# Kernel optimization log

Measured on AMD Instinct MI355X. Metric: run time of the kernel, lower is better.

Reference implementation:

```python
import jax, jax.numpy as jnp
import numpy as np

B, S, E, H, F = 4, 1024, 1024, 16, 4096
D = E // H
DEPTH = 3
EPS_LN = 1e-5
EPS_ENT = 1e-6


def setup_inputs() -> dict:
    key = jax.random.key(0)
    ks = jax.random.split(key, 32)
    def w(k, shp, s=0.02):
        return (jax.random.normal(k, shp) * s).astype(jnp.float32)
    z = lambda *shp: jnp.zeros(shp, jnp.float32)
    inp = {
        'x': jax.random.normal(ks[0], (B, S, E), jnp.float32),
        # self-referential attention
        'sr_w': w(ks[1], (E, E)), 'sr_b': z(E),
        'q_w': w(ks[2], (E, E)), 'q_b': z(E),
        'k_w': w(ks[3], (E, E)), 'k_b': z(E),
        'v_w': w(ks[4], (E, E)), 'v_b': z(E),
        'o_w': w(ks[5], (E, E)), 'o_b': z(E),
        'ref_gate': jnp.float32(0.5),
        # quantum-classical interface
        'c_w': w(ks[6], (E, E)), 'c_b': z(E),
        'qp_w': w(ks[7], (E, E)), 'qp_b': z(E),
        'ig_w': w(ks[8], (2 * E, E)), 'ig_b': z(E),
        'temperature': jnp.float32(1.0),
        # entropy regulator
        'kp_w': w(ks[9], (E, E)), 'kp_b': z(E),
        'ee_w': w(ks[10], (E, 1)), 'ee_b': z(1),
        'eta': jnp.float32(0.1),
        # ffn
        'f1_w': w(ks[11], (E, F)), 'f1_b': z(F),
        'f2_w': w(ks[12], (F, E)), 'f2_b': z(E),
        # layernorms
        'ln1_g': jnp.ones(E, jnp.float32), 'ln1_b': z(E),
        'ln2_g': jnp.ones(E, jnp.float32), 'ln2_b': z(E),
        'ln3_g': jnp.ones(E, jnp.float32), 'ln3_b': z(E),
        # observer
        'obs_w': w(ks[13], (E, E)), 'obs_b': z(E),
        'obs_gate': jnp.float32(0.2),
    }
    return inp


def _lin(x, W, b):
    return x @ W + b


def _ln(x, g, b):
    m = jnp.mean(x, -1, keepdims=True)
    v = jnp.var(x, -1, keepdims=True)
    return (x - m) * jax.lax.rsqrt(v + EPS_LN) * g + b


def _layer(x, p):
    ks = jax.lax.stop_gradient(x)  # knowledge_state = x.detach()
    scale = 1.0 / (D ** 0.5)
    for _ in range(DEPTH):  # fixed small recursion depth
        # --- self-referential attention on norm1(x) ---
        xn = _ln(x, p['ln1_g'], p['ln1_b'])
        xr = xn + p['ref_gate'] * _lin(xn, p['sr_w'], p['sr_b'])
        b, s, _ = xn.shape
        q = _lin(xr, p['q_w'], p['q_b']).reshape(b, s, H, D)
        k = _lin(xr, p['k_w'], p['k_b']).reshape(b, s, H, D)
        v = _lin(xn, p['v_w'], p['v_b']).reshape(b, s, H, D)
        scores = jnp.einsum('bqhd,bkhd->bhqk', q, k) * scale  # [B,H,S,S]
        aw = jax.nn.softmax(scores, axis=-1)
        ao = jnp.einsum('bhqk,bkhd->bqhd', aw, v).reshape(b, s, E)
        quantum = _lin(ao, p['o_w'], p['o_b'])
        # --- FFN on norm2(x) (dropout = identity, eval mode) ---
        xn2 = _ln(x, p['ln2_g'], p['ln2_b'])
        h = jax.nn.gelu(_lin(xn2, p['f1_w'], p['f1_b']), approximate=False)
        classical = _lin(h, p['f2_w'], p['f2_b'])
        # --- quantum-classical interface ---
        c_proj = _lin(classical, p['c_w'], p['c_b'])
        q_proj = _lin(quantum, p['qp_w'], p['qp_b'])
        gate = jax.nn.sigmoid(_lin(jnp.concatenate([c_proj, q_proj], -1), p['ig_w'], p['ig_b']))
        sim = jnp.einsum('bqe,bke->bqk', c_proj, q_proj) / (E ** 0.5)  # [B,S,S]
        attw = jax.nn.softmax(sim / p['temperature'], axis=-1)
        transfer = jnp.einsum('bqk,bke->bqe', attw, quantum)
        iface = classical + gate * transfer
        # --- entropy regulator ---
        logp = jax.nn.log_softmax(iface, axis=-1)
        entropy = -jnp.sum(jnp.exp(logp) * logp, -1, keepdims=True)
        neg_entropy = _lin(ks, p['kp_w'], p['kp_b'])
        bal = jax.nn.sigmoid(_lin(iface, p['ee_w'], p['ee_b']))
        regulated = iface + p['eta'] * bal * (neg_entropy / (entropy + EPS_ENT))
        # --- residual + observer feedback + knowledge update ---
        x = x + regulated
        x = x + p['obs_gate'] * _lin(x, p['obs_w'], p['obs_b'])
        ks = ks + 0.1 * (x - ks)
    x = _ln(x, p['ln3_g'], p['ln3_b'])
    return x, ks


def reference(x, sr_w, sr_b, q_w, q_b, k_w, k_b, v_w, v_b, o_w, o_b, ref_gate,
              c_w, c_b, qp_w, qp_b, ig_w, ig_b, temperature,
              kp_w, kp_b, ee_w, ee_b, eta,
              f1_w, f1_b, f2_w, f2_b,
              ln1_g, ln1_b, ln2_g, ln2_b, ln3_g, ln3_b,
              obs_w, obs_b, obs_gate):
    p = dict(sr_w=sr_w, sr_b=sr_b, q_w=q_w, q_b=q_b, k_w=k_w, k_b=k_b,
             v_w=v_w, v_b=v_b, o_w=o_w, o_b=o_b, ref_gate=ref_gate,
             c_w=c_w, c_b=c_b, qp_w=qp_w, qp_b=qp_b, ig_w=ig_w, ig_b=ig_b,
             temperature=temperature, kp_w=kp_w, kp_b=kp_b, ee_w=ee_w, ee_b=ee_b,
             eta=eta, f1_w=f1_w, f1_b=f1_b, f2_w=f2_w, f2_b=f2_b,
             ln1_g=ln1_g, ln1_b=ln1_b, ln2_g=ln2_g, ln2_b=ln2_b,
             ln3_g=ln3_g, ln3_b=ln3_b, obs_w=obs_w, obs_b=obs_b, obs_gate=obs_gate)
    return _layer(x, p)
```

## Files before the change

kernel.cpp:

```cpp
#include <hip/hip_runtime.h>
#include <hip/hip_bf16.h>
#include <cmath>


typedef unsigned short u16;
typedef short v8s __attribute__((ext_vector_type(8)));
typedef float v4f __attribute__((ext_vector_type(4)));
typedef unsigned short u16x4 __attribute__((ext_vector_type(4)));

#define DEV __device__ __forceinline__

DEV float b2f(u16 u) { return __uint_as_float(((unsigned int)u) << 16); }
DEV u16 f2b(float f) {
    unsigned int x = __float_as_uint(f);
    return (u16)((x + 0x7fffu + ((x >> 16) & 1u)) >> 16);
}
DEV bool badf(float f) { return ((__float_as_uint(f) >> 23) & 0xFF) == 0xFF; }

DEV void async16(const void* g, void* l) {
    __builtin_amdgcn_global_load_lds((const __attribute__((address_space(1))) void*)g,
                                     (__attribute__((address_space(3))) void*)l, 16, 0, 0);
}

struct InArr { const void* p[37]; int n[37]; };
struct BJobs { int si[20]; int off[20]; int n[20]; };
struct GJ2 { const u16* jA; const u16* jB; const u16* jbias; u16* jout; };

#define CLS_CAP 131072

__global__ void reset_k(int* diag, int* cnt) {
    if (threadIdx.x == 0) *diag = 0x7FFFFFFF;
    if (threadIdx.x < 80) cnt[threadIdx.x] = 0;
}

__global__ void classify_k(InArr A, int* cnt) {
    int i = blockIdx.y;
    int n = A.n[i];
    if (n <= 1) return;
    const u16* q = (const u16*)A.p[i];
    long pairs = n >> 1;
    int wild = 0, pz = 0;
    if (pairs > (long)CLS_CAP) {
        long chunk = CLS_CAP / gridDim.x;
        long p0 = (long)blockIdx.x * (pairs / gridDim.x);
        for (long j = p0 + threadIdx.x; j < p0 + chunk; j += blockDim.x) {
            u16 w0 = q[2 * j], w1 = q[2 * j + 1];
            wild += ((w0 & 0x7FFF) >= 0x5000) + ((w1 & 0x7FFF) >= 0x5000);
            pz += (w0 == 0 && w1 >= 0x3000 && w1 <= 0x4100) ? 1 : 0;
        }
    } else {
        long stride = (long)gridDim.x * blockDim.x;
        for (long j = (long)blockIdx.x * blockDim.x + threadIdx.x; j < pairs; j += stride) {
            u16 w0 = q[2 * j], w1 = q[2 * j + 1];
            wild += ((w0 & 0x7FFF) >= 0x5000) + ((w1 & 0x7FFF) >= 0x5000);
            pz += (w0 == 0 && w1 >= 0x3000 && w1 <= 0x4100) ? 1 : 0;
        }
    }
#pragma unroll
    for (int off = 1; off < 64; off <<= 1) {
        wild += __shfl_xor(wild, off);
        pz += __shfl_xor(pz, off);
    }
    if ((threadIdx.x & 63) == 0) {
        atomicAdd(&cnt[2 * i], wild);
        atomicAdd(&cnt[2 * i + 1], pz);
    }
}

__global__ void finalize_k(InArr A, const int* cnt, int* flags) {
    int i = threadIdx.x;
    if (i < 37) {
        int n = A.n[i];
        int f = 0;
        if (n > 1) {
            long pairs = (long)n >> 1;
            long wthr, pthr;
            if (pairs > (long)CLS_CAP) { wthr = (2L * CLS_CAP) >> 6; pthr = (long)CLS_CAP >> 2; }
            else { wthr = (long)n >> 6; pthr = (long)n >> 3; }
            f = (cnt[2 * i] > wthr) || (cnt[2 * i + 1] > pthr);
        }
        flags[i] = f;
    }
}

DEV float dec_scalar(const u16* p) {
    float bf = b2f(p[0]);
    if (bf > 0.0009765625f && bf < 8.0f) return bf;
    unsigned int w = (((unsigned int)p[1]) << 16) | (unsigned int)p[0];
    return __uint_as_float(w);
}

__global__ void decode_scalars_k(const u16* rg, const u16* tp, const u16* et,
                                 const u16* og, float* out)
{
    if (threadIdx.x == 0 && blockIdx.x == 0) {
        out[0] = dec_scalar(rg);
        out[1] = dec_scalar(tp);
        out[2] = dec_scalar(et);
        out[3] = dec_scalar(og);
    }
}

__global__ void cvt1d_k(InArr A, BJobs J, const int* flags, u16* BIA) {
    int j = blockIdx.y;
    int n = J.n[j];
    int si = J.si[j];
    const void* src = A.p[si];
    u16* dst = BIA + (long)J.off[j] * 1024;
    int f = flags[si];
    int stride = gridDim.x * blockDim.x;
    for (int i = blockIdx.x * blockDim.x + threadIdx.x; i < n; i += stride) {
        dst[i] = f ? f2b(((const float*)src)[i]) : ((const u16*)src)[i];
    }
}

__global__ void chk_scal_k(const float* scal, int* diag) {
    if (threadIdx.x == 0) {
        for (int i = 0; i < 4; i++) {
            float v = scal[i];
            if (!(v > 0.f && v < 8.f)) atomicMin(diag, 3);
        }
    }
}

__global__ void fin32_k(float* out, long n4, const int* diag) {
    long stride = (long)gridDim.x * blockDim.x;
    long i0 = (long)blockIdx.x * blockDim.x + threadIdx.x;
    v4f* o4 = (v4f*)out;
    for (long i = i0; i < n4; i += stride) {
        v4f v = o4[i];
        bool b = false;
#pragma unroll
        for (int j = 0; j < 4; j++) b |= badf(v[j]);
        if (b) {
#pragma unroll
            for (int j = 0; j < 4; j++) if (badf(v[j])) v[j] = 0.f;
            o4[i] = v;
        }
    }
    if (i0 == 0) {
        int d = *diag;
        if (d != 0x7FFFFFFF) out[0] = 200.f + 4.f * (float)(d < 70 ? d : 70);
    }
}

__global__ void small_k(float* out, int code) {
    if (threadIdx.x == 0 && blockIdx.x == 0) out[0] = 900.f + 4.f * code;
}

__global__ __launch_bounds__(256) void f2c_k(const float* __restrict__ a, const float* __restrict__ b,
                                             const u16* __restrict__ bias, u16* __restrict__ out,
                                             int stage, int* __restrict__ diag)
{
    long i0 = ((long)blockIdx.x * 256 + threadIdx.x) * 4;
    v4f va = *(const v4f*)(a + i0);
    v4f vb = *(const v4f*)(b + i0);
    int colb = (int)(i0 & 1023);
    bool bad = false;
    u16x4 o;
#pragma unroll
    for (int j = 0; j < 4; j++) {
        float r = va[j] + vb[j] + b2f(bias[colb + j]);
        bad |= badf(r);
        o[j] = f2b(r);
    }
    *(u16x4*)(out + i0) = o;
    if (__ballot(bad) && (threadIdx.x & 63) == 0) atomicMin(diag, stage);
}

__global__ __launch_bounds__(256) void igc_k(const float* __restrict__ a, const float* __restrict__ b,
                                             const u16* __restrict__ bias, u16* __restrict__ out,
                                             int stage, int* __restrict__ diag)
{
    long i0 = ((long)blockIdx.x * 256 + threadIdx.x) * 4;
    v4f va = *(const v4f*)(a + i0);
    v4f vb = *(const v4f*)(b + i0);
    int colb = (int)(i0 & 1023);
    bool bad = false;
    u16x4 o;
#pragma unroll
    for (int j = 0; j < 4; j++) {
        float r = 1.f / (1.f + expf(-(va[j] + vb[j] + b2f(bias[colb + j]))));
        bad |= badf(r);
        o[j] = f2b(r);
    }
    *(u16x4*)(out + i0) = o;
    if (__ballot(bad) && (threadIdx.x & 63) == 0) atomicMin(diag, stage);
}

template <int EPI>
__global__ __launch_bounds__(512) void gemm_bt(
    const u16* __restrict__ A, int lda, long sA,
    const u16* __restrict__ A2, int ksplit,
    const u16* __restrict__ Bt, int ldb, long sB,
    const u16* __restrict__ bias,
    u16* __restrict__ obf, float* __restrict__ of32, int ldc, long sC,
    int K,
    const float* __restrict__ scp,
    const u16* __restrict__ aux,
    float* __restrict__ xaux, float* __restrict__ ksf, u16* __restrict__ ksb,
    float* __restrict__ kso,
    GJ2 J2,
    int stage, int* __restrict__ diag)
{
    __shared__ __align__(16) u16 As[128 * 64];
    __shared__ __align__(16) u16 Bs[128 * 64];
    const int tid = threadIdx.x;
    const int w = tid >> 6, l = tid & 63;
    const int lr = l & 15, lq = l >> 4;

    const int gx = gridDim.x, gy = gridDim.y;
    const int nwg = gx * gy * (int)gridDim.z;
    int flat = blockIdx.x + gx * (blockIdx.y + gy * blockIdx.z);
    int qq = nwg >> 3, rr = nwg & 7;
    int xcd = flat & 7, loc = flat >> 3;
    int nf = (xcd < rr ? xcd * (qq + 1) : rr * (qq + 1) + (xcd - rr) * qq) + loc;
    const int bx = nf % gx;
    int tmp = nf / gx;
    const int by = tmp % gy;
    int z = tmp / gy;

    const u16* Aj = A; const u16* Bj = Bt; const u16* biasj = bias; u16* obfj = obf;
    float* of32j = of32;
    if (J2.jA) {
        if (z == 1) {
            Aj = J2.jA; Bj = J2.jB; biasj = J2.jbias;
            if (EPI == 8) of32j = (float*)J2.jout; else obfj = J2.jout;
        }
        z = 0;
    }

    const int m0 = by * 128, n0 = bx * 128;
    const u16* Az = Aj + (long)z * sA;
    const u16* Bz = Bj + (long)z * sB;
    const int wm = (w >> 2) * 64, wn = (w & 3) * 32;

    v4f zero4 = {0.f, 0.f, 0.f, 0.f};
    v4f acc[4][2];
#pragma unroll
    for (int i = 0; i < 4; i++)
#pragma unroll
        for (int j = 0; j < 2; j++) acc[i][j] = zero4;

    const int swz = lr & 7;
    const int c0s = (lq ^ swz) << 3;
    const int c1s = ((lq + 4) ^ swz) << 3;
    for (int k0 = 0; k0 < K; k0 += 64) {
        __syncthreads();
        const u16* Ab = (k0 < ksplit) ? (Az + k0) : (A2 + (k0 - ksplit));
#pragma unroll
        for (int p = 0; p < 2; p++) {
            int c = p * 512 + tid;
            int row = c >> 3;
            int sc = ((c & 7) ^ (row & 7)) * 8;
            async16(Ab + (long)(m0 + row) * lda + sc, (char*)As + p * 8192 + w * 1024);
            async16(Bz + (long)(n0 + row) * ldb + k0 + sc, (char*)Bs + p * 8192 + w * 1024);
        }
        __syncthreads();
        v8s av0[4], av1[4], bv0[2], bv1[2];
#pragma unroll
        for (int mi = 0; mi < 4; mi++) {
            const u16* Ar = As + ((wm + mi * 16 + lr) << 6);
            av0[mi] = *(const v8s*)(Ar + c0s);
            av1[mi] = *(const v8s*)(Ar + c1s);
        }
#pragma unroll
        for (int ni = 0; ni < 2; ni++) {
            const u16* Br = Bs + ((wn + ni * 16 + lr) << 6);
            bv0[ni] = *(const v8s*)(Br + c0s);
            bv1[ni] = *(const v8s*)(Br + c1s);
        }
#pragma unroll
        for (int mi = 0; mi < 4; mi++)
#pragma unroll
            for (int ni = 0; ni < 2; ni++)
                acc[mi][ni] = __builtin_amdgcn_mfma_f32_16x16x32_bf16(av0[mi], bv0[ni], acc[mi][ni], 0, 0, 0);
#pragma unroll
        for (int mi = 0; mi < 4; mi++)
#pragma unroll
            for (int ni = 0; ni < 2; ni++)
                acc[mi][ni] = __builtin_amdgcn_mfma_f32_16x16x32_bf16(av1[mi], bv1[ni], acc[mi][ni], 0, 0, 0);
    }

    float gsv = 0.f;
    if (EPI == 4 || EPI == 5 || EPI == 6) gsv = scp[0];
    if (EPI == 4) gsv = fmaxf(gsv, 1e-8f);
    bool bad = false;
#pragma unroll
    for (int mi = 0; mi < 4; mi++) {
        int row = m0 + wm + mi * 16 + lq * 4;
#pragma unroll
        for (int ni = 0; ni < 2; ni++) {
            int col = n0 + wn + ni * 16 + lr;
            float bb = biasj ? b2f(biasj[col]) : 0.f;
#pragma unroll
            for (int r = 0; r < 4; r++) {
                float v = acc[mi][ni][r] + bb;
                if (EPI == 6 || EPI == 7) {
                    long rbase = (long)(row + r) * 1024;
                    float res;
                    if (col < 1024) {
                        if (EPI == 6) res = b2f(aux[rbase + col]) + gsv * v;
                        else res = v * 0.125f;
                        bad |= badf(res);
                        obfj[rbase + col] = f2b(res);
                    } else {
                        res = v;
                        bad |= badf(res);
                        J2.jout[rbase + col - 1024] = f2b(res);
                    }
                } else {
                    long idx = (long)z * sC + (long)(row + r) * ldc + col;
                    float res = v;
                    if (EPI == 2) res = 0.5f * v * (1.f + erff(v * 0.70710678118654752f));
                    else if (EPI == 3) res = 1.f / (1.f + expf(-v));
                    else if (EPI == 4) res = v * (0.03125f / gsv);
                    else if (EPI == 5) {
                        float xv = xaux[idx];
                        float nx = xv + gsv * v;
                        xaux[idx] = nx;
                        float kv = ksf[idx];
                        float kn = kv + 0.1f * (nx - kv);
                        ksf[idx] = kn;
                        ksb[idx] = f2b(kn);
                        if (kso) kso[idx] = kn;
                        bad |= badf(kn);
                        res = nx;
                    }
                    bad |= badf(res);
                    if (obfj) obfj[idx] = f2b(res);
                    if (of32j) of32j[idx] = res;
                }
            }
        }
    }
    if (__ballot(bad) && l == 0) atomicMin(diag, stage);
}

__global__ __launch_bounds__(256) void flash_k(
    const u16* __restrict__ q, const u16* __restrict__ k, const u16* __restrict__ v,
    u16* __restrict__ ao, int stage, int* __restrict__ diag)
{
    __shared__ __align__(16) u16 Ks[2 * 64 * 64];
    __shared__ __align__(16) u16 Vt[64 * 64];
    __shared__ __align__(16) u16 Pw[4 * 16 * 64];
    const int tid = threadIdx.x, w = tid >> 6, l = tid & 63;
    const int lr = l & 15, lq = l >> 4;
    const int flat = blockIdx.x + (blockIdx.y << 4);
    const int xcd = flat & 7, loc = flat >> 3;
    const int bh = xcd * 8 + (loc >> 4);
    const int q0 = (loc & 15) * 64;
    const int b = bh >> 4, h = bh & 15;
    const long rowbase = (long)b * 1024;
    const int h64 = h * 64;

    const u16* Qp = q + (rowbase + q0 + w * 16 + lr) * 1024 + h64;
    v8s aq0 = *(const v8s*)(Qp + lq * 8);
    v8s aq1 = *(const v8s*)(Qp + 32 + lq * 8);

    v4f zero4 = {0.f, 0.f, 0.f, 0.f};
    v4f oacc[4];
    float m_r[4], l_r[4];
#pragma unroll
    for (int i = 0; i < 4; i++) { oacc[i] = zero4; m_r[i] = -INFINITY; l_r[i] = 0.f; }

    const int ss = lr & 7;
    const int colk = (lq ^ ss) << 3;
    u16* Pp = Pw + w * (16 * 64);

    const int c0 = tid, c1 = 256 + tid;
    const int row0 = c0 >> 3, cc0 = (c0 & 7) * 8;
    const int row1 = c1 >> 3, cc1 = (c1 & 7) * 8;
    const int sl0 = ((c0 & 7) ^ (row0 & 7)) * 8;
    const int sl1 = ((c1 & 7) ^ (row1 & 7)) * 8;
    int vt0[8], vt1[8];
#pragma unroll
    for (int j = 0; j < 8; j++) {
        int d0 = cc0 + j, g0 = (d0 & 7) ^ ((d0 >> 3) & 7);
        vt0[j] = ((d0 << 6) + row0) ^ (g0 << 3);
        int d1 = cc1 + j, g1 = (d1 & 7) ^ ((d1 >> 3) & 7);
        vt1[j] = ((d1 << 6) + row1) ^ (g1 << 3);
    }
    const u16* kc0 = k + (rowbase + row0) * 1024 + h64 + sl0;
    const u16* kc1 = k + (rowbase + row1) * 1024 + h64 + sl1;
    const u16* vc0 = v + (rowbase + row0) * 1024 + h64 + cc0;
    const u16* vc1 = v + (rowbase + row1) * 1024 + h64 + cc1;

    async16(kc0, (char*)Ks + w * 1024);
    async16(kc1, (char*)Ks + 4096 + w * 1024);
    v8s vv0 = *(const v8s*)vc0;
    v8s vv1 = *(const v8s*)vc1;
    v8s vvn0 = vv0, vvn1 = vv1;
    int cur = 0;

    for (int kt = 0; kt < 16; kt++) {
        __syncthreads();
        const long koff = (long)(kt + 1) << 16;
        if (kt < 15) {
            int nb = (cur ^ 1) * 8192;
            async16(kc0 + koff, (char*)Ks + nb + w * 1024);
            async16(kc1 + koff, (char*)Ks + nb + 4096 + w * 1024);
            vvn0 = *(const v8s*)(vc0 + koff);
            vvn1 = *(const v8s*)(vc1 + koff);
        }
        const u16* Kb = Ks + cur * 4096;

        v4f s[4];
#pragma unroll
        for (int nt = 0; nt < 4; nt++) {
            const u16* Kr = Kb + ((nt * 16 + lr) << 6);
            v8s b0 = *(const v8s*)(Kr + colk);
            v8s b1 = *(const v8s*)(Kr + (colk ^ 32));
            v4f t = zero4;
            t = __builtin_amdgcn_mfma_f32_16x16x32_bf16(aq0, b0, t, 0, 0, 0);
            t = __builtin_amdgcn_mfma_f32_16x16x32_bf16(aq1, b1, t, 0, 0, 0);
            s[nt] = t;
        }
#pragma unroll
        for (int r = 0; r < 4; r++) {
            float mx = fmaxf(fmaxf(s[0][r], s[1][r]), fmaxf(s[2][r], s[3][r]));
#pragma unroll
            for (int off = 1; off < 16; off <<= 1) mx = fmaxf(mx, __shfl_xor(mx, off));
            float mn = fmaxf(m_r[r], mx);
            float al = __expf(m_r[r] - mn);
            float rs = 0.f;
            int qrow = lq * 4 + r;
            int pbase = qrow << 6;
            int pswz = (qrow & 7) << 3;
#pragma unroll
            for (int nt = 0; nt < 4; nt++) {
                float pv = __expf(s[nt][r] - mn);
                rs += pv;
                Pp[pbase + ((nt * 16 + lr) ^ pswz)] = f2b(pv);
            }
#pragma unroll
            for (int off = 1; off < 16; off <<= 1) rs += __shfl_xor(rs, off);
            l_r[r] = l_r[r] * al + rs;
            m_r[r] = mn;
#pragma unroll
            for (int nt = 0; nt < 4; nt++) oacc[nt][r] *= al;
        }
#pragma unroll
        for (int j = 0; j < 8; j++) {
            Vt[vt0[j]] = (u16)vv0[j];
            Vt[vt1[j]] = (u16)vv1[j];
        }
        __syncthreads();
        const u16* Pr = Pp + (lr << 6);
        v8s pa0 = *(const v8s*)(Pr + colk);
        v8s pa1 = *(const v8s*)(Pr + (colk ^ 32));
#pragma unroll
        for (int nt = 0; nt < 4; nt++) {
            const u16* Vr = Vt + ((nt * 16 + lr) << 6);
            int gv = (ss ^ (2 * nt + (lr >> 3))) << 3;
            int colv = (lq << 3) ^ gv;
            v8s vb0 = *(const v8s*)(Vr + colv);
            v8s vb1 = *(const v8s*)(Vr + (colv ^ 32));
            oacc[nt] = __builtin_amdgcn_mfma_f32_16x16x32_bf16(pa0, vb0, oacc[nt], 0, 0, 0);
            oacc[nt] = __builtin_amdgcn_mfma_f32_16x16x32_bf16(pa1, vb1, oacc[nt], 0, 0, 0);
        }
        vv0 = vvn0; vv1 = vvn1;
        cur ^= 1;
    }
    bool bad = false;
#pragma unroll
    for (int r = 0; r < 4; r++) {
        float inv = 1.f / l_r[r];
#pragma unroll
        for (int nt = 0; nt < 4; nt++) {
            float val = oacc[nt][r] * inv;
            bad |= badf(val);
            ao[(rowbase + q0 + w * 16 + lq * 4 + r) * 1024 + h64 + nt * 16 + lr] = f2b(val);
        }
    }
    if (__ballot(bad) && l == 0) atomicMin(diag, stage);
}

template <int F32OUT>
__global__ __launch_bounds__(256) void ln_k(const float* __restrict__ x,
                                            const u16* __restrict__ g, const u16* __restrict__ bt,
                                            u16* __restrict__ outb, float* __restrict__ outf,
                                            int stage, int* __restrict__ diag)
{
    __shared__ float red[8];
    int row = blockIdx.x, t = threadIdx.x, w = t >> 6;
    const float* xr = x + (long)row * 1024;
    float v[4], s = 0.f, sq = 0.f;
#pragma unroll
    for (int i = 0; i < 4; i++) { v[i] = xr[i * 256 + t]; s += v[i]; sq += v[i] * v[i]; }
#pragma unroll
    for (int off = 1; off < 64; off <<= 1) { s += __shfl_xor(s, off); sq += __shfl_xor(sq, off); }
    if ((t & 63) == 0) { red[w] = s; red[4 + w] = sq; }
    __syncthreads();
    float S = red[0] + red[1] + red[2] + red[3];
    float SQ = red[4] + red[5] + red[6] + red[7];
    float mean = S * (1.f / 1024.f);
    float var = fmaxf(SQ * (1.f / 1024.f) - mean * mean, 0.f);
    float rs = rsqrtf(var + 1e-5f);
    bool bad = false;
#pragma unroll
    for (int i = 0; i < 4; i++) {
        int e = i * 256 + t;
        float r = (v[i] - mean) * rs * b2f(g[e]) + b2f(bt[e]);
        bad |= badf(r);
        if (F32OUT) outf[(long)row * 1024 + e] = r;
        else outb[(long)row * 1024 + e] = f2b(r);
    }
    if (__ballot(bad) && (t & 63) == 0) atomicMin(diag, stage);
}

__global__ __launch_bounds__(256) void rowfuse_k(
    const u16* __restrict__ cls, const u16* __restrict__ gate, const float* __restrict__ tr,
    const u16* __restrict__ ne, const u16* __restrict__ eew, const u16* __restrict__ eeb,
    const float* __restrict__ eta_p, float* __restrict__ xbuf, u16* __restrict__ x1b,
    int stage, int* __restrict__ diag)
{
    __shared__ float red[16];
    int row = blockIdx.x, t = threadIdx.x, w = t >> 6;
    long base = (long)row * 1024;
    float ifc[4];
#pragma unroll
    for (int i = 0; i < 4; i++) {
        int e = i * 256 + t;
        ifc[i] = b2f(cls[base + e]) + b2f(gate[base + e]) * tr[base + e];
    }
    float mx = fmaxf(fmaxf(ifc[0], ifc[1]), fmaxf(ifc[2], ifc[3]));
#pragma unroll
    for (int off = 1; off < 64; off <<= 1) mx = fmaxf(mx, __shfl_xor(mx, off));
    if ((t & 63) == 0) red[w] = mx;
    __syncthreads();
    float MX = fmaxf(fmaxf(red[0], red[1]), fmaxf(red[2], red[3]));
    float s1 = 0.f, s2 = 0.f, dot = 0.f;
#pragma unroll
    for (int i = 0; i < 4; i++) {
        int e = i * 256 + t;
        float ex = expf(ifc[i] - MX);
        s1 += ex; s2 += ex * ifc[i]; dot += ifc[i] * b2f(eew[e]);
    }
#pragma unroll
    for (int off = 1; off < 64; off <<= 1) {
        s1 += __shfl_xor(s1, off); s2 += __shfl_xor(s2, off); dot += __shfl_xor(dot, off);
    }
    if ((t & 63) == 0) { red[4 + w] = s1; red[8 + w] = s2; red[12 + w] = dot; }
    __syncthreads();
    float S1 = red[4] + red[5] + red[6] + red[7];
    float S2 = red[8] + red[9] + red[10] + red[11];
    float DT = red[12] + red[13] + red[14] + red[15];
    float logZ = MX + logf(S1);
    float ent = logZ - S2 / S1;
    float bal = 1.f / (1.f + expf(-(DT + b2f(eeb[0]))));
    float fac = eta_p[0] * bal / (ent + 1e-6f);
    bool bad = false;
#pragma unroll
    for (int i = 0; i < 4; i++) {
        int e = i * 256 + t;
        float rg = ifc[i] + fac * b2f(ne[base + e]);
        float x1 = xbuf[base + e] + rg;
        bad |= badf(x1);
        xbuf[base + e] = x1;
        x1b[base + e] = f2b(x1);
    }
    if (__ballot(bad) && (t & 63) == 0) atomicMin(diag, stage);
}

__global__ __launch_bounds__(256) void softmax_k(const float* __restrict__ sim, u16* __restrict__ out,
                                                 int stage, int* __restrict__ diag)
{
    __shared__ float red[8];
    int row = blockIdx.x, t = threadIdx.x, w = t >> 6;
    long base = (long)row * 1024;
    float v[4];
#pragma unroll
    for (int i = 0; i < 4; i++) v[i] = sim[base + i * 256 + t];
    float mx = fmaxf(fmaxf(v[0], v[1]), fmaxf(v[2], v[3]));
#pragma unroll
    for (int off = 1; off < 64; off <<= 1) mx = fmaxf(mx, __shfl_xor(mx, off));
    if ((t & 63) == 0) red[w] = mx;
    __syncthreads();
    float MX = fmaxf(fmaxf(red[0], red[1]), fmaxf(red[2], red[3]));
    float s = 0.f;
#pragma unroll
    for (int i = 0; i < 4; i++) { v[i] = expf(v[i] - MX); s += v[i]; }
#pragma unroll
    for (int off = 1; off < 64; off <<= 1) s += __shfl_xor(s, off);
    if ((t & 63) == 0) red[4 + w] = s;
    __syncthreads();
    float inv = 1.f / (red[4] + red[5] + red[6] + red[7]);
    bool bad = false;
#pragma unroll
    for (int i = 0; i < 4; i++) {
        float o = v[i] * inv;
        bad |= badf(o);
        out[base + i * 256 + t] = f2b(o);
    }
    if (__ballot(bad) && (t & 63) == 0) atomicMin(diag, stage);
}

__global__ void transpose_ft_k(const void* __restrict__ in, u16* __restrict__ out,
                               int R, int C, const int* __restrict__ flags, int idx,
                               int* __restrict__ diag)
{
    __shared__ u16 tile[32][33];
    int f = flags[idx];
    int x = blockIdx.x * 32 + threadIdx.x;
    int y0 = blockIdx.y * 32;
#pragma unroll
    for (int j = 0; j < 4; j++) {
        long src = (long)(y0 + threadIdx.y + j * 8) * C + x;
        tile[threadIdx.y + j * 8][threadIdx.x] =
            f ? f2b(((const float*)in)[src]) : ((const u16*)in)[src];
    }
    __syncthreads();
    int ox = y0 + threadIdx.x;
    int oy0 = blockIdx.x * 32;
    bool bad = false;
#pragma unroll
    for (int j = 0; j < 4; j++) {
        u16 u = tile[threadIdx.x][threadIdx.y + j * 8];
        bad |= ((u & 0x7FFF) >= 0x7F80);
        out[(long)(oy0 + threadIdx.y + j * 8) * R + ox] = u;
    }
    if (__ballot(bad) && ((threadIdx.y * 32 + threadIdx.x) & 63) == 0) atomicMin(diag, 2);
}

__global__ void transpose_k(const u16* __restrict__ in, u16* __restrict__ out,
                            int R, int C, long sIn, long sOut)
{
    __shared__ u16 tile[32][33];
    int z = blockIdx.z;
    in += (long)z * sIn; out += (long)z * sOut;
    int x = blockIdx.x * 32 + threadIdx.x;
    int y0 = blockIdx.y * 32;
#pragma unroll
    for (int j = 0; j < 4; j++)
        tile[threadIdx.y + j * 8][threadIdx.x] = in[(long)(y0 + threadIdx.y + j * 8) * C + x];
    __syncthreads();
    int ox = y0 + threadIdx.x;
    int oy0 = blockIdx.x * 32;
#pragma unroll
    for (int j = 0; j < 4; j++)
        out[(long)(oy0 + threadIdx.y + j * 8) * R + ox] = tile[threadIdx.x][threadIdx.y + j * 8];
}

__global__ __launch_bounds__(256) void init_k(const void* __restrict__ xin, const int* __restrict__ flags,
                                              float* __restrict__ xbuf,
                                              float* __restrict__ ksf, u16* __restrict__ ksb,
                                              int* __restrict__ diag)
{
    int t = threadIdx.x;
    int f = flags[0];
    long base = (long)blockIdx.x * 1024;
    bool bad = false;
#pragma unroll
    for (int i = 0; i < 4; i++) {
        long idx = base + i * 256 + t;
        float xv = f ? ((const float*)xin)[idx] : b2f(((const u16*)xin)[idx]);
        bad |= badf(xv);
        xbuf[idx] = xv; ksf[idx] = xv; ksb[idx] = f2b(xv);
    }
    if (__ballot(bad) && (t & 63) == 0) atomicMin(diag, 1);
}

extern "C" void kernel_launch(void* const* d_in, const int* in_sizes, int n_in,
                              void* d_out, int out_size, void* d_ws, size_t ws_size,
                              hipStream_t stream)
{
    const size_t MB = 1u << 20;
    float* outf = (float*)d_out;
    if (ws_size < 192 * MB) {
        int code = (int)(ws_size >> 25); if (code > 9) code = 9;
        small_k<<<1, 64, 0, stream>>>(outf, code);
        return;
    }
    const u16* s_refg = (const u16*)d_in[11];
    const u16* s_temp = (const u16*)d_in[18];
    const u16* s_eta  = (const u16*)d_in[23];
    const u16* s_obsg = (const u16*)d_in[36];

    InArr IA;
    for (int i = 0; i < 37; i++) { IA.p[i] = d_in[i]; IA.n[i] = (i < n_in) ? in_sizes[i] : 0; }

    char* ws = (char*)d_ws;
    u16* srT  = (u16*)(ws + 0 * MB);
    u16* vT   = (u16*)(ws + 2 * MB);
    u16* qT   = (u16*)(ws + 4 * MB);
    u16* kT   = (u16*)(ws + 6 * MB);
    u16* oT   = (u16*)(ws + 8 * MB);
    u16* cT   = (u16*)(ws + 10 * MB);
    u16* qpT  = (u16*)(ws + 12 * MB);
    u16* kpT  = (u16*)(ws + 14 * MB);
    u16* obsT = (u16*)(ws + 16 * MB);
    u16* igT  = (u16*)(ws + 18 * MB);
    u16* f1T  = (u16*)(ws + 22 * MB);
    u16* f2T  = (u16*)(ws + 30 * MB);
    float* scal = (float*)(ws + 38 * MB);
    int* diag  = (int*)(ws + 38 * MB + 64);
    int* flags = (int*)(ws + 38 * MB + 128);
    int* cnt   = (int*)(ws + 38 * MB + 512);
    u16* BIA   = (u16*)(ws + 38 * MB + 8192);
    u16* c_bsr = BIA + 0*1024,  *c_bv = BIA + 1*1024;
    u16* c_bq  = BIA + 2*1024,  *c_bk = BIA + 3*1024;
    u16* c_bo  = BIA + 4*1024,  *c_bc = BIA + 5*1024;
    u16* c_bqp = BIA + 6*1024,  *c_big = BIA + 7*1024, *c_bkp = BIA + 8*1024;
    u16* c_bobs= BIA + 9*1024,  *c_bf2 = BIA + 10*1024;
    u16* c_g1  = BIA + 11*1024, *c_be1 = BIA + 12*1024;
    u16* c_g2  = BIA + 13*1024, *c_be2 = BIA + 14*1024;
    u16* c_g3  = BIA + 15*1024, *c_be3 = BIA + 16*1024;
    u16* c_eew = BIA + 17*1024, *c_eeb = BIA + 18*1024;
    u16* c_bf1 = BIA + 19*1024;
    float* xbuf = (float*)(ws + 40 * MB);
    float* ksf  = (float*)(ws + 56 * MB);
    u16* ksb    = (u16*)(ws + 72 * MB);
    u16* xn     = (u16*)(ws + 80 * MB);
    u16* xn2    = (u16*)(ws + 88 * MB);
    u16* xr     = (u16*)(ws + 96 * MB);
    u16* qb     = (u16*)(ws + 104 * MB);
    u16* kb     = (u16*)(ws + 112 * MB);
    u16* vb     = (u16*)(ws + 120 * MB);
    u16* aob    = (u16*)(ws + 128 * MB);
    u16* quant  = (u16*)(ws + 136 * MB);
    u16* hb     = (u16*)(ws + 144 * MB);
    float* simf = (float*)(ws + 144 * MB);
    float* trf  = (float*)(ws + 160 * MB);
    u16* clsb   = (u16*)(ws + 176 * MB);
    u16* neb    = (u16*)(ws + 184 * MB);
    float* f2pa = (float*)(ws + 104 * MB);
    float* f2pb = (float*)(ws + 120 * MB);
    float* igpa = (float*)(ws + 144 * MB);
    float* igpb = (float*)(ws + 160 * MB);
    u16* quantT = xn;
    u16* cpb = qb;  u16* qpb = kb;  u16* gateb = vb;  u16* attw = aob;  u16* x1b = xr;

    const long BS1 = 1024L * 1024L;
    const int KBIG = 1 << 30;
    dim3 tb(32, 8), blk(256), gblk(512);
    GJ2 J0 = {nullptr, nullptr, nullptr, nullptr};

    auto G = [&](int epi, int gx, int gy, int gz,
                 const u16* A, int lda, long sA, const u16* A2, int ksp,
                 const u16* Bt, int ldb, long sB, const u16* bias,
                 u16* obf, float* of32, int ldc, long sC, int K,
                 const float* scp, const u16* aux, float* xa, float* kf, u16* kb2, float* kso,
                 GJ2 J2, int stg) {
        dim3 grid(gx, gy, gz);
        switch (epi) {
            case 0: gemm_bt<0><<<grid, gblk, 0, stream>>>(A, lda, sA, A2, ksp, Bt, ldb, sB, bias, obf, of32, ldc, sC, K, scp, aux, xa, kf, kb2, kso, J2, stg, diag); break;
            case 2: gemm_bt<2><<<grid, gblk, 0, stream>>>(A, lda, sA, A2, ksp, Bt, ldb, sB, bias, obf, of32, ldc, sC, K, scp, aux, xa, kf, kb2, kso, J2, stg, diag); break;
            case 3: gemm_bt<3><<<grid, gblk, 0, stream>>>(A, lda, sA, A2, ksp, Bt, ldb, sB, bias, obf, of32, ldc, sC, K, scp, aux, xa, kf, kb2, kso, J2, stg, diag); break;
            case 4: gemm_bt<4><<<grid, gblk, 0, stream>>>(A, lda, sA, A2, ksp, Bt, ldb, sB, bias, obf, of32, ldc, sC, K, scp, aux, xa, kf, kb2, kso, J2, stg, diag); break;
            case 5: gemm_bt<5><<<grid, gblk, 0, stream>>>(A, lda, sA, A2, ksp, Bt, ldb, sB, bias, obf, of32, ldc, sC, K, scp, aux, xa, kf, kb2, kso, J2, stg, diag); break;
            case 6: gemm_bt<6><<<grid, gblk, 0, stream>>>(A, lda, sA, A2, ksp, Bt, ldb, sB, bias, obf, of32, ldc, sC, K, scp, aux, xa, kf, kb2, kso, J2, stg, diag); break;
            case 7: gemm_bt<7><<<grid, gblk, 0, stream>>>(A, lda, sA, A2, ksp, Bt, ldb, sB, bias, obf, of32, ldc, sC, K, scp, aux, xa, kf, kb2, kso, J2, stg, diag); break;
            case 8: gemm_bt<8><<<grid, gblk, 0, stream>>>(A, lda, sA, A2, ksp, Bt, ldb, sB, bias, obf, of32, ldc, sC, K, scp, aux, xa, kf, kb2, kso, J2, stg, diag); break;
        }
    };

    reset_k<<<1, 256, 0, stream>>>(diag, cnt);
    classify_k<<<dim3(64, 37), blk, 0, stream>>>(IA, cnt);
    finalize_k<<<1, 64, 0, stream>>>(IA, cnt, flags);
    decode_scalars_k<<<1, 64, 0, stream>>>(s_refg, s_temp, s_eta, s_obsg, scal);
    BJobs BJ = {
        {2, 8, 4, 6, 10, 13, 15, 17, 20, 35, 27, 28, 29, 30, 31, 32, 33, 21, 22, 25},
        {0, 1, 2, 3, 4, 5, 6, 7, 8, 9, 10, 11, 12, 13, 14, 15, 16, 17, 18, 19},
        {1024,1024,1024,1024,1024,1024,1024,1024,1024,1024,1024,1024,1024,1024,1024,1024,1024,1024,1,4096}
    };
    cvt1d_k<<<dim3(4, 20), blk, 0, stream>>>(IA, BJ, flags, BIA);
    struct WT { int idx; u16* dst; long n; int R, C, gx, gy; };
    WT wts[12] = {
        {1, srT, 1048576, 1024, 1024, 32, 32},  {7, vT, 1048576, 1024, 1024, 32, 32},
        {3, qT, 1048576, 1024, 1024, 32, 32},   {5, kT, 1048576, 1024, 1024, 32, 32},
        {9, oT, 1048576, 1024, 1024, 32, 32},   {12, cT, 1048576, 1024, 1024, 32, 32},
        {14, qpT, 1048576, 1024, 1024, 32, 32}, {19, kpT, 1048576, 1024, 1024, 32, 32},
        {34, obsT, 1048576, 1024, 1024, 32, 32},
        {16, igT, 2097152, 2048, 1024, 32, 64},
        {24, f1T, 4194304, 1024, 4096, 128, 32},
        {26, f2T, 4194304, 4096, 1024, 32, 128},
    };
    for (int i = 0; i < 12; i++) {
        transpose_ft_k<<<dim3(wts[i].gx, wts[i].gy, 1), tb, 0, stream>>>(
            d_in[wts[i].idx], wts[i].dst, wts[i].R, wts[i].C, flags, wts[i].idx, diag);
    }
    init_k<<<4096, blk, 0, stream>>>(d_in[0], flags, xbuf, ksf, ksb, diag);
    chk_scal_k<<<1, 64, 0, stream>>>(scal, diag);

    for (int it = 0; it < 3; it++) {
        int sb = 4 + it * 20;
        ln_k<0><<<4096, blk, 0, stream>>>(xbuf, c_g1, c_be1, xn, nullptr, sb + 0, diag);
        GJ2 Jsrv = {nullptr, nullptr, nullptr, vb};
        G(6, 16, 32, 1, xn, 1024, 0, nullptr, KBIG, srT, 1024, 0, c_bsr, xr, nullptr, 1024, 0, 1024, scal + 0, xn, nullptr, nullptr, nullptr, nullptr, Jsrv, sb + 1);
        GJ2 Jqk = {nullptr, nullptr, nullptr, kb};
        G(7, 16, 32, 1, xr, 1024, 0, nullptr, KBIG, qT, 1024, 0, c_bq, qb, nullptr, 1024, 0, 1024, nullptr, nullptr, nullptr, nullptr, nullptr, nullptr, Jqk, sb + 2);
        flash_k<<<dim3(16, 64), blk, 0, stream>>>(qb, kb, vb, aob, sb + 5, diag);
        GJ2 Jokp = {ksb, kpT, c_bkp, neb};
        G(0, 8, 32, 2, aob, 1024, 0, nullptr, KBIG, oT, 1024, 0, c_bo, quant, nullptr, 1024, 0, 1024, nullptr, nullptr, nullptr, nullptr, nullptr, nullptr, Jokp, sb + 6);
        transpose_k<<<dim3(32, 32, 4), tb, 0, stream>>>(quant, quantT, 1024, 1024, BS1, BS1);
        ln_k<0><<<4096, blk, 0, stream>>>(xbuf, c_g2, c_be2, xn2, nullptr, sb + 7, diag);
        G(2, 32, 32, 1, xn2, 1024, 0, nullptr, KBIG, f1T, 1024, 0, c_bf1, hb, nullptr, 4096, 0, 1024, nullptr, nullptr, nullptr, nullptr, nullptr, nullptr, J0, sb + 8);
        G(8, 8, 32, 2, hb, 4096, 2048, nullptr, KBIG, f2T, 4096, 2048, nullptr, nullptr, f2pa, 1024, 4194304, 2048, nullptr, nullptr, nullptr, nullptr, nullptr, nullptr, J0, sb + 9);
        f2c_k<<<4096, blk, 0, stream>>>(f2pa, f2pb, c_bf2, clsb, sb + 9, diag);
        GJ2 Jcqp = {quant, qpT, c_bqp, qpb};
        G(0, 8, 32, 2, clsb, 1024, 0, nullptr, KBIG, cT, 1024, 0, c_bc, cpb, nullptr, 1024, 0, 1024, nullptr, nullptr, nullptr, nullptr, nullptr, nullptr, Jcqp, sb + 10);
        GJ2 Jig = {qpb, igT + 1024, nullptr, (u16*)igpb};
        G(8, 8, 32, 2, cpb, 1024, 0, nullptr, KBIG, igT, 2048, 0, nullptr, nullptr, igpa, 1024, 0, 1024, nullptr, nullptr, nullptr, nullptr, nullptr, nullptr, Jig, sb + 12);
        igc_k<<<4096, blk, 0, stream>>>(igpa, igpb, c_big, gateb, sb + 12, diag);
        G(4, 8, 8, 4, cpb, 1024, BS1, nullptr, KBIG, qpb, 1024, BS1, nullptr, nullptr, simf, 1024, BS1, 1024, scal + 1, nullptr, nullptr, nullptr, nullptr, nullptr, J0, sb + 14);
        softmax_k<<<4096, blk, 0, stream>>>(simf, attw, sb + 15, diag);
        G(0, 8, 8, 4, attw, 1024, BS1, nullptr, KBIG, quantT, 1024, BS1, nullptr, nullptr, trf, 1024, BS1, 1024, nullptr, nullptr, nullptr, nullptr, nullptr, nullptr, J0, sb + 16);
        rowfuse_k<<<4096, blk, 0, stream>>>(clsb, gateb, trf, neb, c_eew, c_eeb, scal + 2, xbuf, x1b, sb + 17, diag);
        float* kso = (it == 2) ? (outf + 4194304) : nullptr;
        G(5, 8, 32, 1, x1b, 1024, 0, nullptr, KBIG, obsT, 1024, 0, c_bobs, nullptr, nullptr, 1024, 0, 1024, scal + 3, nullptr, xbuf, ksf, ksb, kso, J0, sb + 18);
    }
    ln_k<1><<<4096, blk, 0, stream>>>(xbuf, c_g3, c_be3, nullptr, outf, 70, diag);
    fin32_k<<<1024, blk, 0, stream>>>(outf, 2097152, diag);
}
```

Before: 1.634 ms.

## Split-K the batched similarity and transfer GEMMs and merge both layernorms

The two per-batch 1024x1024x1024 GEMMs (similarity and attention-weighted transfer) were launched with only 4 z-slices of 64 tiles each. They now split K into two halves through the dual-job mechanism, which doubles the grid to 8 z-slices and writes fp32 partials. The temperature scaling moves into softmax, which sums the partials, and rowfuse sums the transfer partials. The two layernorms of x are fused into one kernel that reads x once and writes both normalized outputs. The trade-off is extra fp32 partial traffic to write and reread, and generalized z-splitting logic in the GEMM.

```diff
diff --git a/kernel.cpp b/kernel.cpp
--- a/kernel.cpp
+++ b/kernel.cpp
@@ -223,11 +223,12 @@
     const u16* Aj = A; const u16* Bj = Bt; const u16* biasj = bias; u16* obfj = obf;
     float* of32j = of32;
     if (J2.jA) {
-        if (z == 1) {
+        int jzs = (int)gridDim.z >> 1;
+        if (z >= jzs) {
             Aj = J2.jA; Bj = J2.jB; biasj = J2.jbias;
             if (EPI == 8) of32j = (float*)J2.jout; else obfj = J2.jout;
-        }
-        z = 0;
+            z -= jzs;
+        }
     }
 
     const int m0 = by * 128, n0 = bx * 128;
@@ -283,8 +284,7 @@
     }
 
     float gsv = 0.f;
-    if (EPI == 4 || EPI == 5 || EPI == 6) gsv = scp[0];
-    if (EPI == 4) gsv = fmaxf(gsv, 1e-8f);
+    if (EPI == 5 || EPI == 6) gsv = scp[0];
     bool bad = false;
 #pragma unroll
     for (int mi = 0; mi < 4; mi++) {
@@ -313,8 +313,6 @@
                     long idx = (long)z * sC + (long)(row + r) * ldc + col;
                     float res = v;
                     if (EPI == 2) res = 0.5f * v * (1.f + erff(v * 0.70710678118654752f));
-                    else if (EPI == 3) res = 1.f / (1.f + expf(-v));
-                    else if (EPI == 4) res = v * (0.03125f / gsv);
                     else if (EPI == 5) {
                         float xv = xaux[idx];
                         float nx = xv + gsv * v;
@@ -509,8 +507,44 @@
     if (__ballot(bad) && (t & 63) == 0) atomicMin(diag, stage);
 }
 
+__global__ __launch_bounds__(256) void ln12_k(const float* __restrict__ x,
+                                              const u16* __restrict__ g1, const u16* __restrict__ b1,
+                                              const u16* __restrict__ g2, const u16* __restrict__ b2,
+                                              u16* __restrict__ out1, u16* __restrict__ out2,
+                                              int stage, int* __restrict__ diag)
+{
+    __shared__ float red[8];
+    int row = blockIdx.x, t = threadIdx.x, w = t >> 6;
+    const float* xr = x + (long)row * 1024;
+    float v[4], s = 0.f, sq = 0.f;
+#pragma unroll
+    for (int i = 0; i < 4; i++) { v[i] = xr[i * 256 + t]; s += v[i]; sq += v[i] * v[i]; }
+#pragma unroll
+    for (int off = 1; off < 64; off <<= 1) { s += __shfl_xor(s, off); sq += __shfl_xor(sq, off); }
+    if ((t & 63) == 0) { red[w] = s; red[4 + w] = sq; }
+    __syncthreads();
+    float S = red[0] + red[1] + red[2] + red[3];
+    float SQ = red[4] + red[5] + red[6] + red[7];
+    float mean = S * (1.f / 1024.f);
+    float var = fmaxf(SQ * (1.f / 1024.f) - mean * mean, 0.f);
+    float rs = rsqrtf(var + 1e-5f);
+    bool bad = false;
+#pragma unroll
+    for (int i = 0; i < 4; i++) {
+        int e = i * 256 + t;
+        float nv = (v[i] - mean) * rs;
+        float r1 = nv * b2f(g1[e]) + b2f(b1[e]);
+        float r2 = nv * b2f(g2[e]) + b2f(b2[e]);
+        bad |= badf(r1) | badf(r2);
+        out1[(long)row * 1024 + e] = f2b(r1);
+        out2[(long)row * 1024 + e] = f2b(r2);
+    }
+    if (__ballot(bad) && (t & 63) == 0) atomicMin(diag, stage);
+}
+
 __global__ __launch_bounds__(256) void rowfuse_k(
-    const u16* __restrict__ cls, const u16* __restrict__ gate, const float* __restrict__ tr,
+    const u16* __restrict__ cls, const u16* __restrict__ gate,
+    const float* __restrict__ tra, const float* __restrict__ trb,
     const u16* __restrict__ ne, const u16* __restrict__ eew, const u16* __restrict__ eeb,
     const float* __restrict__ eta_p, float* __restrict__ xbuf, u16* __restrict__ x1b,
     int stage, int* __restrict__ diag)
@@ -522,7 +556,7 @@
 #pragma unroll
     for (int i = 0; i < 4; i++) {
         int e = i * 256 + t;
-        ifc[i] = b2f(cls[base + e]) + b2f(gate[base + e]) * tr[base + e];
+        ifc[i] = b2f(cls[base + e]) + b2f(gate[base + e]) * (tra[base + e] + trb[base + e]);
     }
     float mx = fmaxf(fmaxf(ifc[0], ifc[1]), fmaxf(ifc[2], ifc[3]));
 #pragma unroll
@@ -563,15 +597,17 @@
     if (__ballot(bad) && (t & 63) == 0) atomicMin(diag, stage);
 }
 
-__global__ __launch_bounds__(256) void softmax_k(const float* __restrict__ sim, u16* __restrict__ out,
+__global__ __launch_bounds__(256) void softmax_k(const float* __restrict__ pa, const float* __restrict__ pb,
+                                                 const float* __restrict__ tp, u16* __restrict__ out,
                                                  int stage, int* __restrict__ diag)
 {
     __shared__ float red[8];
     int row = blockIdx.x, t = threadIdx.x, w = t >> 6;
     long base = (long)row * 1024;
+    float sc = 0.03125f / fmaxf(tp[0], 1e-8f);
     float v[4];
 #pragma unroll
-    for (int i = 0; i < 4; i++) v[i] = sim[base + i * 256 + t];
+    for (int i = 0; i < 4; i++) v[i] = (pa[base + i * 256 + t] + pb[base + i * 256 + t]) * sc;
     float mx = fmaxf(fmaxf(v[0], v[1]), fmaxf(v[2], v[3]));
 #pragma unroll
     for (int off = 1; off < 64; off <<= 1) mx = fmaxf(mx, __shfl_xor(mx, off));
@@ -720,14 +756,12 @@
     u16* aob    = (u16*)(ws + 128 * MB);
     u16* quant  = (u16*)(ws + 136 * MB);
     u16* hb     = (u16*)(ws + 144 * MB);
-    float* simf = (float*)(ws + 144 * MB);
-    float* trf  = (float*)(ws + 160 * MB);
     u16* clsb   = (u16*)(ws + 176 * MB);
     u16* neb    = (u16*)(ws + 184 * MB);
     float* f2pa = (float*)(ws + 104 * MB);
     float* f2pb = (float*)(ws + 120 * MB);
-    float* igpa = (float*)(ws + 144 * MB);
-    float* igpb = (float*)(ws + 160 * MB);
+    float* ppa  = (float*)(ws + 144 * MB);
+    float* ppb  = (float*)(ws + 160 * MB);
     u16* quantT = xn;
     u16* cpb = qb;  u16* qpb = kb;  u16* gateb = vb;  u16* attw = aob;  u16* x1b = xr;
 
@@ -746,8 +780,6 @@
         switch (epi) {
             case 0: gemm_bt<0><<<grid, gblk, 0, stream>>>(A, lda, sA, A2, ksp, Bt, ldb, sB, bias, obf, of32, ldc, sC, K, scp, aux, xa, kf, kb2, kso, J2, stg, diag); break;
             case 2: gemm_bt<2><<<grid, gblk, 0, stream>>>(A, lda, sA, A2, ksp, Bt, ldb, sB, bias, obf, of32, ldc, sC, K, scp, aux, xa, kf, kb2, kso, J2, stg, diag); break;
-            case 3: gemm_bt<3><<<grid, gblk, 0, stream>>>(A, lda, sA, A2, ksp, Bt, ldb, sB, bias, obf, of32, ldc, sC, K, scp, aux, xa, kf, kb2, kso, J2, stg, diag); break;
-            case 4: gemm_bt<4><<<grid, gblk, 0, stream>>>(A, lda, sA, A2, ksp, Bt, ldb, sB, bias, obf, of32, ldc, sC, K, scp, aux, xa, kf, kb2, kso, J2, stg, diag); break;
             case 5: gemm_bt<5><<<grid, gblk, 0, stream>>>(A, lda, sA, A2, ksp, Bt, ldb, sB, bias, obf, of32, ldc, sC, K, scp, aux, xa, kf, kb2, kso, J2, stg, diag); break;
             case 6: gemm_bt<6><<<grid, gblk, 0, stream>>>(A, lda, sA, A2, ksp, Bt, ldb, sB, bias, obf, of32, ldc, sC, K, scp, aux, xa, kf, kb2, kso, J2, stg, diag); break;
             case 7: gemm_bt<7><<<grid, gblk, 0, stream>>>(A, lda, sA, A2, ksp, Bt, ldb, sB, bias, obf, of32, ldc, sC, K, scp, aux, xa, kf, kb2, kso, J2, stg, diag); break;
@@ -785,7 +817,7 @@
 
     for (int it = 0; it < 3; it++) {
         int sb = 4 + it * 20;
-        ln_k<0><<<4096, blk, 0, stream>>>(xbuf, c_g1, c_be1, xn, nullptr, sb + 0, diag);
+        ln12_k<<<4096, blk, 0, stream>>>(xbuf, c_g1, c_be1, c_g2, c_be2, xn, xn2, sb + 0, diag);
         GJ2 Jsrv = {nullptr, nullptr, nullptr, vb};
         G(6, 16, 32, 1, xn, 1024, 0, nullptr, KBIG, srT, 1024, 0, c_bsr, xr, nullptr, 1024, 0, 1024, scal + 0, xn, nullptr, nullptr, nullptr, nullptr, Jsrv, sb + 1);
         GJ2 Jqk = {nullptr, nullptr, nullptr, kb};
@@ -794,19 +826,20 @@
         GJ2 Jokp = {ksb, kpT, c_bkp, neb};
         G(0, 8, 32, 2, aob, 1024, 0, nullptr, KBIG, oT, 1024, 0, c_bo, quant, nullptr, 1024, 0, 1024, nullptr, nullptr, nullptr, nullptr, nullptr, nullptr, Jokp, sb + 6);
         transpose_k<<<dim3(32, 32, 4), tb, 0, stream>>>(quant, quantT, 1024, 1024, BS1, BS1);
-        ln_k<0><<<4096, blk, 0, stream>>>(xbuf, c_g2, c_be2, xn2, nullptr, sb + 7, diag);
         G(2, 32, 32, 1, xn2, 1024, 0, nullptr, KBIG, f1T, 1024, 0, c_bf1, hb, nullptr, 4096, 0, 1024, nullptr, nullptr, nullptr, nullptr, nullptr, nullptr, J0, sb + 8);
         G(8, 8, 32, 2, hb, 4096, 2048, nullptr, KBIG, f2T, 4096, 2048, nullptr, nullptr, f2pa, 1024, 4194304, 2048, nullptr, nullptr, nullptr, nullptr, nullptr, nullptr, J0, sb + 9);
         f2c_k<<<4096, blk, 0, stream>>>(f2pa, f2pb, c_bf2, clsb, sb + 9, diag);
         GJ2 Jcqp = {quant, qpT, c_bqp, qpb};
         G(0, 8, 32, 2, clsb, 1024, 0, nullptr, KBIG, cT, 1024, 0, c_bc, cpb, nullptr, 1024, 0, 1024, nullptr, nullptr, nullptr, nullptr, nullptr, nullptr, Jcqp, sb + 10);
-        GJ2 Jig = {qpb, igT + 1024, nullptr, (u16*)igpb};
-        G(8, 8, 32, 2, cpb, 1024, 0, nullptr, KBIG, igT, 2048, 0, nullptr, nullptr, igpa, 1024, 0, 1024, nullptr, nullptr, nullptr, nullptr, nullptr, nullptr, Jig, sb + 12);
-        igc_k<<<4096, blk, 0, stream>>>(igpa, igpb, c_big, gateb, sb + 12, diag);
-        G(4, 8, 8, 4, cpb, 1024, BS1, nullptr, KBIG, qpb, 1024, BS1, nullptr, nullptr, simf, 1024, BS1, 1024, scal + 1, nullptr, nullptr, nullptr, nullptr, nullptr, J0, sb + 14);
-        softmax_k<<<4096, blk, 0, stream>>>(simf, attw, sb + 15, diag);
-        G(0, 8, 8, 4, attw, 1024, BS1, nullptr, KBIG, quantT, 1024, BS1, nullptr, nullptr, trf, 1024, BS1, 1024, nullptr, nullptr, nullptr, nullptr, nullptr, nullptr, J0, sb + 16);
-        rowfuse_k<<<4096, blk, 0, stream>>>(clsb, gateb, trf, neb, c_eew, c_eeb, scal + 2, xbuf, x1b, sb + 17, diag);
+        GJ2 Jig = {qpb, igT + 1024, nullptr, (u16*)ppb};
+        G(8, 8, 32, 2, cpb, 1024, 0, nullptr, KBIG, igT, 2048, 0, nullptr, nullptr, ppa, 1024, 0, 1024, nullptr, nullptr, nullptr, nullptr, nullptr, nullptr, Jig, sb + 12);
+        igc_k<<<4096, blk, 0, stream>>>(ppa, ppb, c_big, gateb, sb + 12, diag);
+        GJ2 Jsim = {cpb + 512, qpb + 512, nullptr, (u16*)ppb};
+        G(8, 8, 8, 8, cpb, 1024, BS1, nullptr, KBIG, qpb, 1024, BS1, nullptr, nullptr, ppa, 1024, BS1, 512, nullptr, nullptr, nullptr, nullptr, nullptr, nullptr, Jsim, sb + 14);
+        softmax_k<<<4096, blk, 0, stream>>>(ppa, ppb, scal + 1, attw, sb + 15, diag);
+        GJ2 Jtrf = {attw + 512, quantT + 512, nullptr, (u16*)ppb};
+        G(8, 8, 8, 8, attw, 1024, BS1, nullptr, KBIG, quantT, 1024, BS1, nullptr, nullptr, ppa, 1024, BS1, 512, nullptr, nullptr, nullptr, nullptr, nullptr, nullptr, Jtrf, sb + 16);
+        rowfuse_k<<<4096, blk, 0, stream>>>(clsb, gateb, ppa, ppb, neb, c_eew, c_eeb, scal + 2, xbuf, x1b, sb + 17, diag);
         float* kso = (it == 2) ? (outf + 4194304) : nullptr;
         G(5, 8, 32, 1, x1b, 1024, 0, nullptr, KBIG, obsT, 1024, 0, c_bobs, nullptr, nullptr, 1024, 0, 1024, scal + 3, nullptr, xbuf, ksf, ksb, kso, J0, sb + 18);
     }
```

Result: no change. 1.647 ms (+0.8%).
